# Performance work log

Hardware: AMD Instinct MI355X
Metric: run time of the kernel (lower is better)

Reference implementation:

```python
import jax, jax.numpy as jnp
import numpy as np

# ---- FNET: small stride-4 CNN feature extractor (3 -> 64 channels) ----

def _conv(x, w, b, stride, pad):
    y = jax.lax.conv_general_dilated(x, w, (stride, stride), [(pad, pad), (pad, pad)],
                                     dimension_numbers=('NCHW', 'OIHW', 'NCHW'))
    return y + b[None, :, None, None]


def _fnet(x, w1, b1, w2, b2, w3, b3):
    x = jax.nn.relu(_conv(x, w1, b1, 2, 3))   # /2
    x = jax.nn.relu(_conv(x, w2, b2, 2, 1))   # /4
    return _conv(x, w3, b3, 1, 1)             # [N, 64, H/4, W/4]


def _bilinear(feat, u, v):
    # feat: [C, Hf, Wf]; u, v: [D, H, W] pixel coords. Zero padding outside.
    C, Hf, Wf = feat.shape
    u0 = jnp.floor(u); v0 = jnp.floor(v)
    du = u - u0; dv = v - v0
    def gather(ui, vi):
        inb = (ui >= 0) & (ui < Wf) & (vi >= 0) & (vi < Hf)
        uic = jnp.clip(ui, 0, Wf - 1).astype(jnp.int32)
        vic = jnp.clip(vi, 0, Hf - 1).astype(jnp.int32)
        return feat[:, vic, uic] * inb[None].astype(feat.dtype)  # [C, D, H, W]
    f00 = gather(u0, v0);     f01 = gather(u0 + 1, v0)
    f10 = gather(u0, v0 + 1); f11 = gather(u0 + 1, v0 + 1)
    return (f00 * ((1 - du) * (1 - dv))[None] + f01 * (du * (1 - dv))[None]
            + f10 * ((1 - du) * dv)[None] + f11 * (du * dv)[None])


def _magnet_f(ref_img, nghbr_imgs, nghbr_poses, is_valid, cam_intrins, d_center,
              w1, b1, w2, b2, w3, b3):
    B = ref_img.shape[0]
    feat_4 = _fnet(jnp.concatenate([ref_img, nghbr_imgs], axis=0), w1, b1, w2, b2, w3, b3)
    ref_feat = feat_4[:B]                      # [B, C, H4, W4]
    ngh_feat = feat_4[B:]                      # [B*V, C, H4, W4]
    BV = ngh_feat.shape[0]; V = BV // B
    C, H4, W4 = ref_feat.shape[1:]
    D = d_center.shape[1]

    R = nghbr_poses[:, :, :3, :3]              # [B, V, 3, 3]
    t = nghbr_poses[:, :, :3, 3]               # [B, V, 3]
    Kinv = jnp.linalg.inv(cam_intrins)         # [B, 3, 3]

    dt = d_center.dtype
    ys, xs = jnp.meshgrid(jnp.arange(H4, dtype=dt), jnp.arange(W4, dtype=dt), indexing='ij')
    pix = jnp.stack([xs, ys, jnp.ones_like(xs)], 0)          # [3, H4, W4]
    rays = jnp.einsum('bij,jhw->bihw', Kinv, pix)            # [B, 3, H4, W4]
    P = d_center[:, None] * rays[:, :, None]                 # [B, 3, D, H4, W4]
    P_src = jnp.einsum('bvij,bjdhw->bvidhw', R, P) + t[..., None, None, None]
    p = jnp.einsum('bij,bvjdhw->bvidhw', cam_intrins, P_src) # [B, V, 3, D, H4, W4]

    z = p[:, :, 2]
    z_ok = z > 1e-3
    zc = jnp.maximum(z, 1e-3)
    u = p[:, :, 0] / zc
    v = p[:, :, 1] / zc                                      # [B, V, D, H4, W4]
    inb = (u >= 0) & (u <= W4 - 1) & (v >= 0) & (v <= H4 - 1)

    warped = jax.vmap(_bilinear)(ngh_feat,
                                 u.reshape(BV, D, H4, W4),
                                 v.reshape(BV, D, H4, W4))   # [B*V, C, D, H4, W4]
    warped = warped.reshape(B, V, C, D, H4, W4)

    cost = jnp.einsum('bchw,bvcdhw->bvdhw', ref_feat, warped) / C  # [B, V, D, H4, W4]
    mask = (is_valid[:, :, None, None, None] & z_ok & inb).astype(cost.dtype)
    cost_volume = (cost * mask).sum(1) / jnp.maximum(mask.sum(1), 1.0)  # [B, D, H4, W4]
    return cost_volume


def setup_inputs() -> dict:
    B, V, H, W, D, C = 2, 4, 480, 640, 5, 64
    H4, W4 = H // 4, W // 4
    ks = jax.random.split(jax.random.key(0), 12)
    ref_img = jax.random.normal(ks[0], (B, 3, H, W), jnp.float32)
    nghbr_imgs = jax.random.normal(ks[1], (B * V, 3, H, W), jnp.float32)
    # near-identity relative poses with small random translations
    poses = jnp.tile(jnp.eye(4, dtype=jnp.float32), (B, V, 1, 1))
    poses = poses.at[:, :, :3, 3].set(0.05 * jax.random.normal(ks[2], (B, V, 3), jnp.float32))
    is_valid = jnp.ones((B, V), dtype=bool)
    K = jnp.array([[144.0, 0.0, 80.0], [0.0, 144.0, 60.0], [0.0, 0.0, 1.0]], jnp.float32)
    cam_intrins = jnp.tile(K, (B, 1, 1))
    d_center = jax.random.uniform(ks[3], (B, D, H4, W4), jnp.float32, 0.5, 5.0)
    w1 = 0.1 * jax.random.normal(ks[4], (32, 3, 7, 7), jnp.float32); b1 = jnp.zeros((32,), jnp.float32)
    w2 = 0.1 * jax.random.normal(ks[5], (C, 32, 3, 3), jnp.float32); b2 = jnp.zeros((C,), jnp.float32)
    w3 = 0.1 * jax.random.normal(ks[6], (C, C, 3, 3), jnp.float32); b3 = jnp.zeros((C,), jnp.float32)
    return {"ref_img": ref_img, "nghbr_imgs": nghbr_imgs, "nghbr_poses": poses,
            "is_valid": is_valid, "cam_intrins": cam_intrins, "d_center": d_center,
            "w1": w1, "b1": b1, "w2": w2, "b2": b2, "w3": w3, "b3": b3}


def reference(ref_img, nghbr_imgs, nghbr_poses, is_valid, cam_intrins, d_center,
              w1, b1, w2, b2, w3, b3):
    return _magnet_f(ref_img, nghbr_imgs, nghbr_poses, is_valid, cam_intrins, d_center,
                     w1, b1, w2, b2, w3, b3)
```

## Files before the change

kernel.cpp:

```cpp
#include <hip/hip_runtime.h>
#include <hip/hip_bf16.h>

#define B_  2
#define V_  4
#define Hin 480
#define Win 640
#define H2  240
#define W2  320
#define H4  120
#define W4  160
#define C1  32
#define C_  64
#define D_  5
#define NIMG 10
#define HW4 (H4*W4)

#define P1H 242
#define P1W 322
#define P2H 122
#define P2W 162
#define PIH 486
#define PIW 646

typedef __attribute__((ext_vector_type(8))) short short8;
typedef __attribute__((ext_vector_type(4))) float f32x4;

#define OFF_F1HI 0
#define OFF_F1LO 12467840
#define OFF_F2HI 24935680
#define OFF_F2LO 31260160
#define OFF_INHI 24935680
#define OFF_INLO 29645504
#define OFF_F3   0
#define OFF_SAMPW 12467840
#define OFF_SAMPM 15539840
#define OFF_GEOM 37584640
#define OFF_W1P  37584736
#define OFF_W2P  37590880
#define OFF_W3P  37609312

__global__ void packw_kernel(const float* __restrict__ w, ushort* __restrict__ dst,
                             int CI, int NK, int lo_off) {
    int idx = blockIdx.x * 256 + threadIdx.x;
    int total = 4 * NK * 64 * 8;
    if (idx >= total) return;
    int j = idx & 7;
    int lane = (idx >> 3) & 63;
    int s = (idx >> 9) % NK;
    int t = idx / (NK * 512);
    int k = s * 32 + (lane >> 4) * 8 + j;
    int co = t * 16 + (lane & 15);
    int kyx = k / CI;
    int ci  = k % CI;
    int ky = kyx / 3, kx = kyx % 3;
    float val = w[((co * CI + ci) * 3 + ky) * 3 + kx];
    __hip_bfloat16 h = __float2bfloat16(val);
    float hf = __bfloat162float(h);
    __hip_bfloat16 l = __float2bfloat16(val - hf);
    dst[idx]          = *reinterpret_cast<ushort*>(&h);
    dst[lo_off + idx] = *reinterpret_cast<ushort*>(&l);
}

__global__ void packw1_kernel(const float* __restrict__ w, ushort* __restrict__ dst) {
    int idx = blockIdx.x * 256 + threadIdx.x;
    if (idx >= 6144) return;
    int j = idx & 7;
    int lane = (idx >> 3) & 63;
    int s = (idx >> 9) % 6;
    int t = idx / 3072;
    int g = s * 4 + (lane >> 4);
    int co = t * 16 + (lane & 15);
    float val = 0.0f;
    if (g < 21 && j < 7) {
        int ci = g / 7, ky = g % 7;
        val = w[((co * 3 + ci) * 7 + ky) * 7 + j];
    }
    __hip_bfloat16 h = __float2bfloat16(val);
    float hf = __bfloat162float(h);
    __hip_bfloat16 l = __float2bfloat16(val - hf);
    dst[idx]        = *reinterpret_cast<ushort*>(&h);
    dst[6144 + idx] = *reinterpret_cast<ushort*>(&l);
}

__global__ void packin_kernel(const float* __restrict__ ref, const float* __restrict__ ngh,
                              ushort* __restrict__ ihi, ushort* __restrict__ ilo) {
    int idx = blockIdx.x * 256 + threadIdx.x;
    const int tot = NIMG * 3 * PIH * PIW;
    if (idx >= tot) return;
    int x = idx % PIW;
    int r = idx / PIW;
    int y = r % PIH;
    int rc = r / PIH;
    int ci = rc % 3;
    int n  = rc / 3;
    float val = 0.0f;
    int lx = x - 3, ly = y - 3;
    if (lx >= 0 && lx < Win && ly >= 0 && ly < Hin) {
        const float* img = (n < B_) ? (ref + ((size_t)n * 3 + ci) * Hin * Win)
                                    : (ngh + ((size_t)(n - B_) * 3 + ci) * Hin * Win);
        val = img[(size_t)ly * Win + lx];
    }
    __hip_bfloat16 h = __float2bfloat16(val);
    float hf = __bfloat162float(h);
    __hip_bfloat16 l = __float2bfloat16(val - hf);
    ihi[idx] = *reinterpret_cast<ushort*>(&h);
    ilo[idx] = *reinterpret_cast<ushort*>(&l);
}

__global__ void zerob_kernel(ushort* __restrict__ f1hi, ushort* __restrict__ f1lo,
                             ushort* __restrict__ f2hi, ushort* __restrict__ f2lo) {
    const int F1B = 2 * P1W + 2 * (P1H - 2);
    const int F2B = 2 * P2W + 2 * (P2H - 2);
    const int f1tot = NIMG * F1B * C1;
    const int f2tot = NIMG * F2B * C_;
    int idx = blockIdx.x * 256 + threadIdx.x;
    if (idx < f1tot) {
        int c = idx & 31; int r = idx >> 5;
        int n = r / F1B; int bp = r % F1B;
        int y, x;
        if (bp < P1W)            { y = 0;        x = bp; }
        else if (bp < 2*P1W)     { y = P1H - 1;  x = bp - P1W; }
        else if (bp < 2*P1W + (P1H-2)) { y = bp - 2*P1W + 1;   x = 0; }
        else                     { y = bp - 2*P1W - (P1H-2) + 1; x = P1W - 1; }
        size_t o = (((size_t)n * P1H + y) * P1W + x) * C1 + c;
        f1hi[o] = 0; f1lo[o] = 0;
        return;
    }
    idx -= f1tot;
    if (idx < f2tot) {
        int c = idx & 63; int r = idx >> 6;
        int n = r / F2B; int bp = r % F2B;
        int y, x;
        if (bp < P2W)            { y = 0;        x = bp; }
        else if (bp < 2*P2W)     { y = P2H - 1;  x = bp - P2W; }
        else if (bp < 2*P2W + (P2H-2)) { y = bp - 2*P2W + 1;   x = 0; }
        else                     { y = bp - 2*P2W - (P2H-2) + 1; x = P2W - 1; }
        size_t o = (((size_t)n * P2H + y) * P2W + x) * C_ + c;
        f2hi[o] = 0; f2lo[o] = 0;
    }
}

__global__ void geom_kernel(const float* __restrict__ poses,
                            const float* __restrict__ Kmat,
                            float* __restrict__ geom) {
    int i = threadIdx.x;
    if (i >= B_ * V_) return;
    int b = i / V_;
    const float* Kb = Kmat + b * 9;
    float k00=Kb[0],k01=Kb[1],k02=Kb[2];
    float k10=Kb[3],k11=Kb[4],k12=Kb[5];
    float k20=Kb[6],k21=Kb[7],k22=Kb[8];
    float det = k00*(k11*k22-k12*k21) - k01*(k10*k22-k12*k20) + k02*(k10*k21-k11*k20);
    float id = 1.0f / det;
    float ki[9];
    ki[0]=(k11*k22-k12*k21)*id; ki[1]=(k02*k21-k01*k22)*id; ki[2]=(k01*k12-k02*k11)*id;
    ki[3]=(k12*k20-k10*k22)*id; ki[4]=(k00*k22-k02*k20)*id; ki[5]=(k02*k10-k00*k12)*id;
    ki[6]=(k10*k21-k11*k20)*id; ki[7]=(k01*k20-k00*k21)*id; ki[8]=(k00*k11-k01*k10)*id;
    const float* P = poses + i * 16;
    float R[9] = {P[0],P[1],P[2], P[4],P[5],P[6], P[8],P[9],P[10]};
    float t[3] = {P[3],P[7],P[11]};
    float KR[9];
    for (int r = 0; r < 3; r++)
        for (int c = 0; c < 3; c++)
            KR[r*3+c] = Kb[r*3+0]*R[0*3+c] + Kb[r*3+1]*R[1*3+c] + Kb[r*3+2]*R[2*3+c];
    float* g = geom + i * 12;
    for (int r = 0; r < 3; r++)
        for (int c = 0; c < 3; c++)
            g[r*3+c] = KR[r*3+0]*ki[0*3+c] + KR[r*3+1]*ki[1*3+c] + KR[r*3+2]*ki[2*3+c];
    for (int r = 0; r < 3; r++)
        g[9+r] = Kb[r*3+0]*t[0] + Kb[r*3+1]*t[1] + Kb[r*3+2]*t[2];
}

__global__ __launch_bounds__(256) void conv1_mfma(
        const ushort* __restrict__ ihi, const ushort* __restrict__ ilo,
        const ushort* __restrict__ w1p, const float* __restrict__ b1,
        ushort* __restrict__ f1hi, ushort* __restrict__ f1lo) {
    const int lane = threadIdx.x & 63;
    const int wv   = threadIdx.x >> 6;
    const int n    = blockIdx.y;
    const int px0  = blockIdx.x * 64 + wv * 16;
    const int p    = px0 + (lane & 15);
    const int y = p / W2, x = p % W2;
    const int kg = lane >> 4;
    const ushort* ih = ihi + (size_t)n * 3 * PIH * PIW;
    const ushort* il = ilo + (size_t)n * 3 * PIH * PIW;

    f32x4 acc[2] = {};
#pragma unroll
    for (int s = 0; s < 6; s++) {
        const int g = s * 4 + kg;
        short8 ahi = {}, alo = {};
        if (g < 21) {
            const int ci = g / 7, ky = g % 7;
            const size_t off = ((size_t)(ci * PIH + 2 * y + ky)) * PIW + 2 * x;
            ahi = *reinterpret_cast<const short8*>(ih + off);
            alo = *reinterpret_cast<const short8*>(il + off);
        }
#pragma unroll
        for (int t = 0; t < 2; t++) {
            const int widx = ((t * 6 + s) * 64 + lane) * 8;
            short8 bhi = *reinterpret_cast<const short8*>(w1p + widx);
            short8 blo = *reinterpret_cast<const short8*>(w1p + 6144 + widx);
            acc[t] = __builtin_amdgcn_mfma_f32_16x16x32_bf16(ahi, bhi, acc[t], 0, 0, 0);
            acc[t] = __builtin_amdgcn_mfma_f32_16x16x32_bf16(ahi, blo, acc[t], 0, 0, 0);
            acc[t] = __builtin_amdgcn_mfma_f32_16x16x32_bf16(alo, bhi, acc[t], 0, 0, 0);
        }
    }
#pragma unroll
    for (int t = 0; t < 2; t++) {
        const int co = t * 16 + (lane & 15);
        const float bias = b1[co];
#pragma unroll
        for (int j = 0; j < 4; j++) {
            const int pr = px0 + kg * 4 + j;
            const int oy = pr / W2, ox = pr % W2;
            float val = fmaxf(acc[t][j] + bias, 0.0f);
            __hip_bfloat16 h = __float2bfloat16(val);
            float hf = __bfloat162float(h);
            __hip_bfloat16 l = __float2bfloat16(val - hf);
            const size_t o = (((size_t)n * P1H + (oy + 1)) * P1W + (ox + 1)) * C1 + co;
            f1hi[o] = *reinterpret_cast<ushort*>(&h);
            f1lo[o] = *reinterpret_cast<ushort*>(&l);
        }
    }
}

__global__ __launch_bounds__(256) void conv2_mfma(
        const ushort* __restrict__ f1hi, const ushort* __restrict__ f1lo,
        const ushort* __restrict__ w2p, const float* __restrict__ b2,
        ushort* __restrict__ f2hi, ushort* __restrict__ f2lo) {
    const int lane = threadIdx.x & 63;
    const int wv   = threadIdx.x >> 6;
    const int n    = blockIdx.y;
    const int px0  = blockIdx.x * 64 + wv * 16;
    const int p    = px0 + (lane & 15);
    const int y = p / W4, x = p % W4;
    const int kg = lane >> 4;
    const ushort* ihi = f1hi + (size_t)n * P1H * P1W * C1;
    const ushort* ilo = f1lo + (size_t)n * P1H * P1W * C1;

    f32x4 acc[4] = {};
#pragma unroll
    for (int s = 0; s < 9; s++) {
        const int ky = s / 3, kx = s % 3;
        const int off = ((2 * y + ky) * P1W + (2 * x + kx)) * C1 + kg * 8;
        short8 ahi = *reinterpret_cast<const short8*>(ihi + off);
        short8 alo = *reinterpret_cast<const short8*>(ilo + off);
#pragma unroll
        for (int t = 0; t < 4; t++) {
            const int widx = ((t * 9 + s) * 64 + lane) * 8;
            short8 bhi = *reinterpret_cast<const short8*>(w2p + widx);
            short8 blo = *reinterpret_cast<const short8*>(w2p + 18432 + widx);
            acc[t] = __builtin_amdgcn_mfma_f32_16x16x32_bf16(ahi, bhi, acc[t], 0, 0, 0);
            acc[t] = __builtin_amdgcn_mfma_f32_16x16x32_bf16(ahi, blo, acc[t], 0, 0, 0);
            acc[t] = __builtin_amdgcn_mfma_f32_16x16x32_bf16(alo, bhi, acc[t], 0, 0, 0);
        }
    }
    ushort* ohi = f2hi + (size_t)n * P2H * P2W * C_;
    ushort* olo = f2lo + (size_t)n * P2H * P2W * C_;
#pragma unroll
    for (int t = 0; t < 4; t++) {
        const int co = t * 16 + (lane & 15);
        const float bias = b2[co];
#pragma unroll
        for (int j = 0; j < 4; j++) {
            const int pr = px0 + kg * 4 + j;
            const int yy = pr / W4, xx = pr % W4;
            float val = fmaxf(acc[t][j] + bias, 0.0f);
            __hip_bfloat16 h = __float2bfloat16(val);
            float hf = __bfloat162float(h);
            __hip_bfloat16 l = __float2bfloat16(val - hf);
            const size_t o = (((size_t)(yy + 1)) * P2W + (xx + 1)) * C_ + co;
            ohi[o] = *reinterpret_cast<ushort*>(&h);
            olo[o] = *reinterpret_cast<ushort*>(&l);
        }
    }
}

__global__ __launch_bounds__(256) void conv3_mfma(
        const ushort* __restrict__ f2hi, const ushort* __restrict__ f2lo,
        const ushort* __restrict__ w3p, const float* __restrict__ b3,
        float* __restrict__ f3) {
    const int lane = threadIdx.x & 63;
    const int wv   = threadIdx.x >> 6;
    const int n    = blockIdx.y;
    const int px0  = blockIdx.x * 64 + wv * 16;
    const int p    = px0 + (lane & 15);
    const int y = p / W4, x = p % W4;
    const int kg = lane >> 4;
    const ushort* ihi = f2hi + (size_t)n * P2H * P2W * C_;
    const ushort* ilo = f2lo + (size_t)n * P2H * P2W * C_;

    f32x4 acc[4] = {};
#pragma unroll
    for (int s = 0; s < 18; s++) {
        const int kyx = s >> 1;
        const int ky = kyx / 3, kx = kyx % 3;
        const int ci0 = (s & 1) * 32 + kg * 8;
        const int off = ((y + ky) * P2W + (x + kx)) * C_ + ci0;
        short8 ahi = *reinterpret_cast<const short8*>(ihi + off);
        short8 alo = *reinterpret_cast<const short8*>(ilo + off);
#pragma unroll
        for (int t = 0; t < 4; t++) {
            const int widx = ((t * 18 + s) * 64 + lane) * 8;
            short8 bhi = *reinterpret_cast<const short8*>(w3p + widx);
            short8 blo = *reinterpret_cast<const short8*>(w3p + 36864 + widx);
            acc[t] = __builtin_amdgcn_mfma_f32_16x16x32_bf16(ahi, bhi, acc[t], 0, 0, 0);
            acc[t] = __builtin_amdgcn_mfma_f32_16x16x32_bf16(ahi, blo, acc[t], 0, 0, 0);
            acc[t] = __builtin_amdgcn_mfma_f32_16x16x32_bf16(alo, bhi, acc[t], 0, 0, 0);
        }
    }
    float* op = f3 + (size_t)n * H4 * W4 * C_;
#pragma unroll
    for (int t = 0; t < 4; t++) {
        const int co = t * 16 + (lane & 15);
        const float bias = b3[co];
#pragma unroll
        for (int j = 0; j < 4; j++) {
            const int pr = px0 + kg * 4 + j;
            op[(size_t)pr * C_ + co] = acc[t][j] + bias;
        }
    }
}

__global__ void samp_kernel(const float* __restrict__ geom,
                            const float* __restrict__ dc,
                            const int*   __restrict__ valid,
                            f32x4* __restrict__ sw, int* __restrict__ sm) {
    int idx = blockIdx.x * 256 + threadIdx.x;
    if (idx >= B_ * V_ * D_ * HW4) return;
    int hw = idx % HW4;
    int r  = idx / HW4;
    int d = r % D_;  r /= D_;
    int v = r % V_;  int b = r / V_;
    int h = hw / W4, w = hw % W4;

    float dep = dc[((size_t)(b * D_ + d)) * HW4 + hw];
    const float* g = geom + (b * V_ + v) * 12;
    float px = dep * (g[0] * w + g[1] * h + g[2]) + g[9];
    float py = dep * (g[3] * w + g[4] * h + g[5]) + g[10];
    float pz = dep * (g[6] * w + g[7] * h + g[8]) + g[11];
    bool zok = pz > 0.001f;
    float zc = fmaxf(pz, 0.001f);
    float u  = px / zc;
    float vv = py / zc;
    bool inb = (u >= 0.f) && (u <= (float)(W4 - 1)) &&
               (vv >= 0.f) && (vv <= (float)(H4 - 1));
    bool m = zok && inb && (valid[b * V_ + v] != 0);

    f32x4 wgt = {0.f, 0.f, 0.f, 0.f};
    int rec = 0;
    if (m) {
        float u0f = floorf(u), v0f = floorf(vv);
        float du = u - u0f, dv = vv - v0f;
        int u0 = (int)u0f, v0 = (int)v0f;
        int off00 = v0 * W4 + u0;
        int off10 = min(v0 + 1, H4 - 1) * W4 + u0;
        wgt[0] = (1.f - du) * (1.f - dv);
        wgt[1] = du * (1.f - dv);
        wgt[2] = (1.f - du) * dv;
        wgt[3] = du * dv;
        rec = off00 | (off10 << 15) | (1 << 30);
    }
    sw[idx] = wgt;
    sm[idx] = rec;
}

__global__ __launch_bounds__(256) void warpcost_kernel(
        const float* __restrict__ feat,
        const f32x4* __restrict__ sw, const int* __restrict__ sm,
        float* __restrict__ out) {
    const int wave = threadIdx.x >> 6;
    const int lane = threadIdx.x & 63;
    int pid = blockIdx.x * 4 + wave;
    int b = pid / HW4;
    int hw = pid % HW4;

    const float refc = feat[((size_t)b * HW4 + hw) * C_ + lane];

    float accv[D_] = {0.f, 0.f, 0.f, 0.f, 0.f};
    float den[D_]  = {0.f, 0.f, 0.f, 0.f, 0.f};

#pragma unroll
    for (int v = 0; v < V_; v++) {
        const float* fimg = feat + (size_t)(B_ + b * V_ + v) * HW4 * C_;
        const int rbase = ((b * V_ + v) * D_) * HW4 + hw;
#pragma unroll
        for (int d = 0; d < D_; d++) {
            int rec  = sm[rbase + d * HW4];
            f32x4 wv = sw[rbase + d * HW4];
            int off00 = rec & 0x7FFF;
            int off10 = (rec >> 15) & 0x7FFF;
            const float* p0 = fimg + (size_t)off00 * C_ + lane;
            const float* p1 = fimg + (size_t)off10 * C_ + lane;
            accv[d] += p0[0] * wv[0] + p0[C_] * wv[1] + p1[0] * wv[2] + p1[C_] * wv[3];
            den[d]  += (float)((rec >> 30) & 1);
        }
    }

#pragma unroll
    for (int d = 0; d < D_; d++) {
        float s = refc * accv[d];
        for (int off = 32; off > 0; off >>= 1) s += __shfl_xor(s, off, 64);
        if (lane == 0) {
            out[((size_t)b * D_ + d) * HW4 + hw] =
                (s * (1.0f / (float)C_)) / fmaxf(den[d], 1.0f);
        }
    }
}

extern "C" void kernel_launch(void* const* d_in, const int* in_sizes, int n_in,
                              void* d_out, int out_size, void* d_ws, size_t ws_size,
                              hipStream_t stream) {
    const float* ref_img  = (const float*)d_in[0];
    const float* ngh_img  = (const float*)d_in[1];
    const float* poses    = (const float*)d_in[2];
    const int*   is_valid = (const int*)  d_in[3];
    const float* K        = (const float*)d_in[4];
    const float* dc       = (const float*)d_in[5];
    const float* w1 = (const float*)d_in[6];
    const float* b1 = (const float*)d_in[7];
    const float* w2 = (const float*)d_in[8];
    const float* b2 = (const float*)d_in[9];
    const float* w3 = (const float*)d_in[10];
    const float* b3 = (const float*)d_in[11];
    float* out = (float*)d_out;

    float* ws = (float*)d_ws;
    ushort* f1hi = (ushort*)(ws + OFF_F1HI);
    ushort* f1lo = (ushort*)(ws + OFF_F1LO);
    ushort* f2hi = (ushort*)(ws + OFF_F2HI);
    ushort* f2lo = (ushort*)(ws + OFF_F2LO);
    ushort* inhi = (ushort*)(ws + OFF_INHI);
    ushort* inlo = (ushort*)(ws + OFF_INLO);
    float*  f3   = ws + OFF_F3;
    f32x4*  sw   = (f32x4*)(ws + OFF_SAMPW);
    int*    sm   = (int*)  (ws + OFF_SAMPM);
    float*  geom = ws + OFF_GEOM;
    ushort* w1p  = (ushort*)(ws + OFF_W1P);
    ushort* w2p  = (ushort*)(ws + OFF_W2P);
    ushort* w3p  = (ushort*)(ws + OFF_W3P);

    geom_kernel<<<1, 64, 0, stream>>>(poses, K, geom);
    packw1_kernel<<<24, 256, 0, stream>>>(w1, w1p);
    packw_kernel<<<(4*9*64*8 + 255)/256, 256, 0, stream>>>(w2, w2p, C1, 9, 18432);
    packw_kernel<<<(4*18*64*8 + 255)/256, 256, 0, stream>>>(w3, w3p, C_, 18, 36864);
    packin_kernel<<<(NIMG*3*PIH*PIW + 255)/256, 256, 0, stream>>>(ref_img, ngh_img, inhi, inlo);

    conv1_mfma<<<dim3(H2*W2/64, NIMG), 256, 0, stream>>>(inhi, inlo, w1p, b1, f1hi, f1lo);
    {
        const int ztot = NIMG*(2*P1W + 2*(P1H-2))*C1 + NIMG*(2*P2W + 2*(P2H-2))*C_;
        zerob_kernel<<<(ztot + 255)/256, 256, 0, stream>>>(f1hi, f1lo, f2hi, f2lo);
    }
    conv2_mfma<<<dim3(H4*W4/64, NIMG), 256, 0, stream>>>(f1hi, f1lo, w2p, b2, f2hi, f2lo);
    samp_kernel<<<(B_*V_*D_*HW4 + 255)/256, 256, 0, stream>>>(geom, dc, is_valid, sw, sm);
    conv3_mfma<<<dim3(H4*W4/64, NIMG), 256, 0, stream>>>(f2hi, f2lo, w3p, b3, f3);

    warpcost_kernel<<<(B_*HW4)/4, 256, 0, stream>>>(f3, sw, sm, out);
}
```

Before: 438.0 us.

## Process two pixel tiles per wave in conv kernels and swizzle block order

Each wave in the three MFMA conv kernels now computes 32 output pixels instead of 16. The loaded weight fragments are reused across two accumulator sets, which halves weight loads per output and the number of blocks launched. Block indices are remapped through an XCD-style swizzle (swz8) so neighbouring pixel tiles land on the same chiplet, which should improve L2 locality. The cost is more registers per thread (doubled accumulators and A fragments), which may reduce occupancy.

```diff
diff --git a/kernel.cpp b/kernel.cpp
--- a/kernel.cpp
+++ b/kernel.cpp
@@ -38,6 +38,11 @@
 #define OFF_W1P  37584736
 #define OFF_W2P  37590880
 #define OFF_W3P  37609312
+
+__device__ __forceinline__ int swz8(int o, int n) {
+    int x = o & 7, i = o >> 3, q = n >> 3, r = n & 7;
+    return (x < r) ? (x * (q + 1) + i) : (r * (q + 1) + (x - r) * q + i);
+}
 
 __global__ void packw_kernel(const float* __restrict__ w, ushort* __restrict__ dst,
                              int CI, int NK, int lo_off) {
@@ -178,32 +183,41 @@
     const int lane = threadIdx.x & 63;
     const int wv   = threadIdx.x >> 6;
     const int n    = blockIdx.y;
-    const int px0  = blockIdx.x * 64 + wv * 16;
-    const int p    = px0 + (lane & 15);
-    const int y = p / W2, x = p % W2;
+    const int bx   = swz8(blockIdx.x, 600);
+    const int px0  = bx * 128 + wv * 32;
+    const int p0   = px0 + (lane & 15);
+    const int p1   = p0 + 16;
+    const int y0 = p0 / W2, x0 = p0 % W2;
+    const int y1 = p1 / W2, x1 = p1 % W2;
     const int kg = lane >> 4;
     const ushort* ih = ihi + (size_t)n * 3 * PIH * PIW;
     const ushort* il = ilo + (size_t)n * 3 * PIH * PIW;
 
-    f32x4 acc[2] = {};
+    f32x4 acc[2][2] = {};
 #pragma unroll
     for (int s = 0; s < 6; s++) {
         const int g = s * 4 + kg;
-        short8 ahi = {}, alo = {};
+        short8 a0h = {}, a0l = {}, a1h = {}, a1l = {};
         if (g < 21) {
             const int ci = g / 7, ky = g % 7;
-            const size_t off = ((size_t)(ci * PIH + 2 * y + ky)) * PIW + 2 * x;
-            ahi = *reinterpret_cast<const short8*>(ih + off);
-            alo = *reinterpret_cast<const short8*>(il + off);
+            const size_t o0 = ((size_t)(ci * PIH + 2 * y0 + ky)) * PIW + 2 * x0;
+            const size_t o1 = ((size_t)(ci * PIH + 2 * y1 + ky)) * PIW + 2 * x1;
+            a0h = *reinterpret_cast<const short8*>(ih + o0);
+            a0l = *reinterpret_cast<const short8*>(il + o0);
+            a1h = *reinterpret_cast<const short8*>(ih + o1);
+            a1l = *reinterpret_cast<const short8*>(il + o1);
         }
 #pragma unroll
         for (int t = 0; t < 2; t++) {
             const int widx = ((t * 6 + s) * 64 + lane) * 8;
             short8 bhi = *reinterpret_cast<const short8*>(w1p + widx);
             short8 blo = *reinterpret_cast<const short8*>(w1p + 6144 + widx);
-            acc[t] = __builtin_amdgcn_mfma_f32_16x16x32_bf16(ahi, bhi, acc[t], 0, 0, 0);
-            acc[t] = __builtin_amdgcn_mfma_f32_16x16x32_bf16(ahi, blo, acc[t], 0, 0, 0);
-            acc[t] = __builtin_amdgcn_mfma_f32_16x16x32_bf16(alo, bhi, acc[t], 0, 0, 0);
+            acc[t][0] = __builtin_amdgcn_mfma_f32_16x16x32_bf16(a0h, bhi, acc[t][0], 0, 0, 0);
+            acc[t][0] = __builtin_amdgcn_mfma_f32_16x16x32_bf16(a0h, blo, acc[t][0], 0, 0, 0);
+            acc[t][0] = __builtin_amdgcn_mfma_f32_16x16x32_bf16(a0l, bhi, acc[t][0], 0, 0, 0);
+            acc[t][1] = __builtin_amdgcn_mfma_f32_16x16x32_bf16(a1h, bhi, acc[t][1], 0, 0, 0);
+            acc[t][1] = __builtin_amdgcn_mfma_f32_16x16x32_bf16(a1h, blo, acc[t][1], 0, 0, 0);
+            acc[t][1] = __builtin_amdgcn_mfma_f32_16x16x32_bf16(a1l, bhi, acc[t][1], 0, 0, 0);
         }
     }
 #pragma unroll
@@ -211,16 +225,19 @@
         const int co = t * 16 + (lane & 15);
         const float bias = b1[co];
 #pragma unroll
-        for (int j = 0; j < 4; j++) {
-            const int pr = px0 + kg * 4 + j;
-            const int oy = pr / W2, ox = pr % W2;
-            float val = fmaxf(acc[t][j] + bias, 0.0f);
-            __hip_bfloat16 h = __float2bfloat16(val);
-            float hf = __bfloat162float(h);
-            __hip_bfloat16 l = __float2bfloat16(val - hf);
-            const size_t o = (((size_t)n * P1H + (oy + 1)) * P1W + (ox + 1)) * C1 + co;
-            f1hi[o] = *reinterpret_cast<ushort*>(&h);
-            f1lo[o] = *reinterpret_cast<ushort*>(&l);
+        for (int pt = 0; pt < 2; pt++) {
+#pragma unroll
+            for (int j = 0; j < 4; j++) {
+                const int pr = px0 + pt * 16 + kg * 4 + j;
+                const int oy = pr / W2, ox = pr % W2;
+                float val = fmaxf(acc[t][pt][j] + bias, 0.0f);
+                __hip_bfloat16 h = __float2bfloat16(val);
+                float hf = __bfloat162float(h);
+                __hip_bfloat16 l = __float2bfloat16(val - hf);
+                const size_t o = (((size_t)n * P1H + (oy + 1)) * P1W + (ox + 1)) * C1 + co;
+                f1hi[o] = *reinterpret_cast<ushort*>(&h);
+                f1lo[o] = *reinterpret_cast<ushort*>(&l);
+            }
         }
     }
 }
@@ -232,28 +249,37 @@
     const int lane = threadIdx.x & 63;
     const int wv   = threadIdx.x >> 6;
     const int n    = blockIdx.y;
-    const int px0  = blockIdx.x * 64 + wv * 16;
-    const int p    = px0 + (lane & 15);
-    const int y = p / W4, x = p % W4;
+    const int bx   = swz8(blockIdx.x, 150);
+    const int px0  = bx * 128 + wv * 32;
+    const int p0   = px0 + (lane & 15);
+    const int p1   = p0 + 16;
+    const int y0 = p0 / W4, x0 = p0 % W4;
+    const int y1 = p1 / W4, x1 = p1 % W4;
     const int kg = lane >> 4;
     const ushort* ihi = f1hi + (size_t)n * P1H * P1W * C1;
     const ushort* ilo = f1lo + (size_t)n * P1H * P1W * C1;
 
-    f32x4 acc[4] = {};
+    f32x4 acc[4][2] = {};
 #pragma unroll
     for (int s = 0; s < 9; s++) {
         const int ky = s / 3, kx = s % 3;
-        const int off = ((2 * y + ky) * P1W + (2 * x + kx)) * C1 + kg * 8;
-        short8 ahi = *reinterpret_cast<const short8*>(ihi + off);
-        short8 alo = *reinterpret_cast<const short8*>(ilo + off);
+        const int o0 = ((2 * y0 + ky) * P1W + (2 * x0 + kx)) * C1 + kg * 8;
+        const int o1 = ((2 * y1 + ky) * P1W + (2 * x1 + kx)) * C1 + kg * 8;
+        short8 a0h = *reinterpret_cast<const short8*>(ihi + o0);
+        short8 a0l = *reinterpret_cast<const short8*>(ilo + o0);
+        short8 a1h = *reinterpret_cast<const short8*>(ihi + o1);
+        short8 a1l = *reinterpret_cast<const short8*>(ilo + o1);
 #pragma unroll
         for (int t = 0; t < 4; t++) {
             const int widx = ((t * 9 + s) * 64 + lane) * 8;
             short8 bhi = *reinterpret_cast<const short8*>(w2p + widx);
             short8 blo = *reinterpret_cast<const short8*>(w2p + 18432 + widx);
-            acc[t] = __builtin_amdgcn_mfma_f32_16x16x32_bf16(ahi, bhi, acc[t], 0, 0, 0);
-            acc[t] = __builtin_amdgcn_mfma_f32_16x16x32_bf16(ahi, blo, acc[t], 0, 0, 0);
-            acc[t] = __builtin_amdgcn_mfma_f32_16x16x32_bf16(alo, bhi, acc[t], 0, 0, 0);
+            acc[t][0] = __builtin_amdgcn_mfma_f32_16x16x32_bf16(a0h, bhi, acc[t][0], 0, 0, 0);
+            acc[t][0] = __builtin_amdgcn_mfma_f32_16x16x32_bf16(a0h, blo, acc[t][0], 0, 0, 0);
+            acc[t][0] = __builtin_amdgcn_mfma_f32_16x16x32_bf16(a0l, bhi, acc[t][0], 0, 0, 0);
+            acc[t][1] = __builtin_amdgcn_mfma_f32_16x16x32_bf16(a1h, bhi, acc[t][1], 0, 0, 0);
+            acc[t][1] = __builtin_amdgcn_mfma_f32_16x16x32_bf16(a1h, blo, acc[t][1], 0, 0, 0);
+            acc[t][1] = __builtin_amdgcn_mfma_f32_16x16x32_bf16(a1l, bhi, acc[t][1], 0, 0, 0);
         }
     }
     ushort* ohi = f2hi + (size_t)n * P2H * P2W * C_;
@@ -263,16 +289,19 @@
         const int co = t * 16 + (lane & 15);
         const float bias = b2[co];
 #pragma unroll
-        for (int j = 0; j < 4; j++) {
-            const int pr = px0 + kg * 4 + j;
-            const int yy = pr / W4, xx = pr % W4;
-            float val = fmaxf(acc[t][j] + bias, 0.0f);
-            __hip_bfloat16 h = __float2bfloat16(val);
-            float hf = __bfloat162float(h);
-            __hip_bfloat16 l = __float2bfloat16(val - hf);
-            const size_t o = (((size_t)(yy + 1)) * P2W + (xx + 1)) * C_ + co;
-            ohi[o] = *reinterpret_cast<ushort*>(&h);
-            olo[o] = *reinterpret_cast<ushort*>(&l);
+        for (int pt = 0; pt < 2; pt++) {
+#pragma unroll
+            for (int j = 0; j < 4; j++) {
+                const int pr = px0 + pt * 16 + kg * 4 + j;
+                const int yy = pr / W4, xx = pr % W4;
+                float val = fmaxf(acc[t][pt][j] + bias, 0.0f);
+                __hip_bfloat16 h = __float2bfloat16(val);
+                float hf = __bfloat162float(h);
+                __hip_bfloat16 l = __float2bfloat16(val - hf);
+                const size_t o = (((size_t)(yy + 1)) * P2W + (xx + 1)) * C_ + co;
+                ohi[o] = *reinterpret_cast<ushort*>(&h);
+                olo[o] = *reinterpret_cast<ushort*>(&l);
+            }
         }
     }
 }
@@ -284,30 +313,39 @@
     const int lane = threadIdx.x & 63;
     const int wv   = threadIdx.x >> 6;
     const int n    = blockIdx.y;
-    const int px0  = blockIdx.x * 64 + wv * 16;
-    const int p    = px0 + (lane & 15);
-    const int y = p / W4, x = p % W4;
+    const int bx   = swz8(blockIdx.x, 150);
+    const int px0  = bx * 128 + wv * 32;
+    const int p0   = px0 + (lane & 15);
+    const int p1   = p0 + 16;
+    const int y0 = p0 / W4, x0 = p0 % W4;
+    const int y1 = p1 / W4, x1 = p1 % W4;
     const int kg = lane >> 4;
     const ushort* ihi = f2hi + (size_t)n * P2H * P2W * C_;
     const ushort* ilo = f2lo + (size_t)n * P2H * P2W * C_;
 
-    f32x4 acc[4] = {};
+    f32x4 acc[4][2] = {};
 #pragma unroll
     for (int s = 0; s < 18; s++) {
         const int kyx = s >> 1;
         const int ky = kyx / 3, kx = kyx % 3;
         const int ci0 = (s & 1) * 32 + kg * 8;
-        const int off = ((y + ky) * P2W + (x + kx)) * C_ + ci0;
-        short8 ahi = *reinterpret_cast<const short8*>(ihi + off);
-        short8 alo = *reinterpret_cast<const short8*>(ilo + off);
+        const int o0 = ((y0 + ky) * P2W + (x0 + kx)) * C_ + ci0;
+        const int o1 = ((y1 + ky) * P2W + (x1 + kx)) * C_ + ci0;
+        short8 a0h = *reinterpret_cast<const short8*>(ihi + o0);
+        short8 a0l = *reinterpret_cast<const short8*>(ilo + o0);
+        short8 a1h = *reinterpret_cast<const short8*>(ihi + o1);
+        short8 a1l = *reinterpret_cast<const short8*>(ilo + o1);
 #pragma unroll
         for (int t = 0; t < 4; t++) {
             const int widx = ((t * 18 + s) * 64 + lane) * 8;
             short8 bhi = *reinterpret_cast<const short8*>(w3p + widx);
             short8 blo = *reinterpret_cast<const short8*>(w3p + 36864 + widx);
-            acc[t] = __builtin_amdgcn_mfma_f32_16x16x32_bf16(ahi, bhi, acc[t], 0, 0, 0);
-            acc[t] = __builtin_amdgcn_mfma_f32_16x16x32_bf16(ahi, blo, acc[t], 0, 0, 0);
-            acc[t] = __builtin_amdgcn_mfma_f32_16x16x32_bf16(alo, bhi, acc[t], 0, 0, 0);
+            acc[t][0] = __builtin_amdgcn_mfma_f32_16x16x32_bf16(a0h, bhi, acc[t][0], 0, 0, 0);
+            acc[t][0] = __builtin_amdgcn_mfma_f32_16x16x32_bf16(a0h, blo, acc[t][0], 0, 0, 0);
+            acc[t][0] = __builtin_amdgcn_mfma_f32_16x16x32_bf16(a0l, bhi, acc[t][0], 0, 0, 0);
+            acc[t][1] = __builtin_amdgcn_mfma_f32_16x16x32_bf16(a1h, bhi, acc[t][1], 0, 0, 0);
+            acc[t][1] = __builtin_amdgcn_mfma_f32_16x16x32_bf16(a1h, blo, acc[t][1], 0, 0, 0);
+            acc[t][1] = __builtin_amdgcn_mfma_f32_16x16x32_bf16(a1l, bhi, acc[t][1], 0, 0, 0);
         }
     }
     float* op = f3 + (size_t)n * H4 * W4 * C_;
@@ -316,9 +354,12 @@
         const int co = t * 16 + (lane & 15);
         const float bias = b3[co];
 #pragma unroll
-        for (int j = 0; j < 4; j++) {
-            const int pr = px0 + kg * 4 + j;
-            op[(size_t)pr * C_ + co] = acc[t][j] + bias;
+        for (int pt = 0; pt < 2; pt++) {
+#pragma unroll
+            for (int j = 0; j < 4; j++) {
+                const int pr = px0 + pt * 16 + kg * 4 + j;
+                op[(size_t)pr * C_ + co] = acc[t][pt][j] + bias;
+            }
         }
     }
 }
@@ -447,14 +488,14 @@
     packw_kernel<<<(4*18*64*8 + 255)/256, 256, 0, stream>>>(w3, w3p, C_, 18, 36864);
     packin_kernel<<<(NIMG*3*PIH*PIW + 255)/256, 256, 0, stream>>>(ref_img, ngh_img, inhi, inlo);
 
-    conv1_mfma<<<dim3(H2*W2/64, NIMG), 256, 0, stream>>>(inhi, inlo, w1p, b1, f1hi, f1lo);
+    conv1_mfma<<<dim3(H2*W2/128, NIMG), 256, 0, stream>>>(inhi, inlo, w1p, b1, f1hi, f1lo);
     {
         const int ztot = NIMG*(2*P1W + 2*(P1H-2))*C1 + NIMG*(2*P2W + 2*(P2H-2))*C_;
         zerob_kernel<<<(ztot + 255)/256, 256, 0, stream>>>(f1hi, f1lo, f2hi, f2lo);
     }
-    conv2_mfma<<<dim3(H4*W4/64, NIMG), 256, 0, stream>>>(f1hi, f1lo, w2p, b2, f2hi, f2lo);
+    conv2_mfma<<<dim3(H4*W4/128, NIMG), 256, 0, stream>>>(f1hi, f1lo, w2p, b2, f2hi, f2lo);
     samp_kernel<<<(B_*V_*D_*HW4 + 255)/256, 256, 0, stream>>>(geom, dc, is_valid, sw, sm);
-    conv3_mfma<<<dim3(H4*W4/64, NIMG), 256, 0, stream>>>(f2hi, f2lo, w3p, b3, f3);
+    conv3_mfma<<<dim3(H4*W4/128, NIMG), 256, 0, stream>>>(f2hi, f2lo, w3p, b3, f3);
 
     warpcost_kernel<<<(B_*HW4)/4, 256, 0, stream>>>(f3, sw, sm, out);
 }
```

After: 407.5 us. -7.0%, faster.
